# Performance work log

Measured on AMD Instinct MI355X. Metric: run time of the kernel, lower is better.

Reference implementation:

```python
import jax, jax.numpy as jnp
import numpy as np

EPS = 1e-5
K = 5


def _bn(h, g, b):
    # BatchNorm1d in training mode: batch stats over all dims except channels.
    ax = tuple(range(h.ndim - 1))
    mu = jnp.mean(h, axis=ax, keepdims=True)
    var = jnp.var(h, axis=ax, keepdims=True)
    return g * (h - mu) * jax.lax.rsqrt(var + EPS) + b


def _block(x, w, b, g, be):
    # Lin -> ReLU -> BN, as in MLP() helper
    return _bn(jax.nn.relu(x @ w + b), g, be)


def _knn_idx(x, k):
    # x: [B, P, D]; k nearest per point (includes self at distance 0)
    sq = jnp.sum(x * x, axis=-1)
    d2 = sq[:, :, None] + sq[:, None, :] - 2.0 * jnp.einsum('bpd,bqd->bpq', x, x)
    return jax.lax.top_k(-d2, k)[1]  # [B, P, k]


def _edge_conv(x, k, mlp_fn):
    # DynamicEdgeConv: recompute kNN graph on current features, gather
    # neighbor/center pairs, per-edge MLP on [x_i, x_j - x_i], max-aggregate.
    idx = _knn_idx(x, k)                                   # [B,P,k]
    xj = jax.vmap(lambda xb, ib: xb[ib])(x, idx)           # [B,P,k,D]
    xi = jnp.broadcast_to(x[:, :, None, :], xj.shape)
    e = jnp.concatenate([xi, xj - xi], axis=-1)            # [B,P,k,2D]
    return jnp.max(mlp_fn(e), axis=2)                      # max aggr -> [B,P,C]


def dec_forward(pos,
                c1w0, c1b0, c1g0, c1e0,
                c1w1, c1b1, c1g1, c1e1,
                c1w2, c1b2, c1g2, c1e2,
                c2w, c2b, c2g, c2e,
                l1w, l1b, l1g, l1e,
                m1w, m1b, m1g, m1e,
                m2w, m2b, m2g, m2e,
                m3w, m3b):
    mlp1 = lambda e: _block(_block(_block(e, c1w0, c1b0, c1g0, c1e0),
                                   c1w1, c1b1, c1g1, c1e1),
                            c1w2, c1b2, c1g2, c1e2)
    x1 = _edge_conv(pos, K, mlp1)                          # [B,P,64]
    x2 = _edge_conv(x1, K, lambda e: _block(e, c2w, c2b, c2g, c2e))  # [B,P,128]
    h = _block(jnp.concatenate([x1, x2], axis=-1), l1w, l1b, l1g, l1e)  # [B,P,1024]
    p = jnp.max(h, axis=1)                                 # global_max_pool -> [B,1024]
    p = _block(p, m1w, m1b, m1g, m1e)                      # dropout omitted (eval)
    p = _block(p, m2w, m2b, m2g, m2e)
    return p @ m3w + m3b                                   # [B, n_classes]


def setup_inputs() -> dict:
    key = jax.random.key(0)
    ks = jax.random.split(key, 12)
    B, P = 16, 2048

    def w(k, shape):
        return 0.05 * jax.random.normal(k, shape, jnp.float32)

    z = lambda c: jnp.zeros((c,), jnp.float32)
    o = lambda c: jnp.ones((c,), jnp.float32)

    d = {
        'pos': jax.random.normal(ks[0], (B, P, 3), jnp.float32),
        'c1w0': w(ks[1], (6, 64)), 'c1b0': z(64), 'c1g0': o(64), 'c1e0': z(64),
        'c1w1': w(ks[2], (64, 64)), 'c1b1': z(64), 'c1g1': o(64), 'c1e1': z(64),
        'c1w2': w(ks[3], (64, 64)), 'c1b2': z(64), 'c1g2': o(64), 'c1e2': z(64),
        'c2w': w(ks[4], (128, 128)), 'c2b': z(128), 'c2g': o(128), 'c2e': z(128),
        'l1w': w(ks[5], (192, 1024)), 'l1b': z(1024), 'l1g': o(1024), 'l1e': z(1024),
        'm1w': w(ks[6], (1024, 512)), 'm1b': z(512), 'm1g': o(512), 'm1e': z(512),
        'm2w': w(ks[7], (512, 256)), 'm2b': z(256), 'm2g': o(256), 'm2e': z(256),
        'm3w': w(ks[8], (256, 2)), 'm3b': z(2),
    }
    return d


def reference(pos,
              c1w0, c1b0, c1g0, c1e0,
              c1w1, c1b1, c1g1, c1e1,
              c1w2, c1b2, c1g2, c1e2,
              c2w, c2b, c2g, c2e,
              l1w, l1b, l1g, l1e,
              m1w, m1b, m1g, m1e,
              m2w, m2b, m2g, m2e,
              m3w, m3b):
    return dec_forward(pos,
                       c1w0, c1b0, c1g0, c1e0,
                       c1w1, c1b1, c1g1, c1e1,
                       c1w2, c1b2, c1g2, c1e2,
                       c2w, c2b, c2g, c2e,
                       l1w, l1b, l1g, l1e,
                       m1w, m1b, m1g, m1e,
                       m2w, m2b, m2g, m2e,
                       m3w, m3b)
```

## Files before the change

kernel.cpp:

```cpp
#include <hip/hip_runtime.h>
#include <cmath>

constexpr int B = 16, P = 2048, KNN = 5;
constexpr int BP = B * P;
constexpr int E = BP * KNN;
constexpr float EPS = 1e-5f;
constexpr int QC2 = 4;

constexpr int ST0 = 0;
constexpr int ST1 = 128;
constexpr int ST2 = 256;
constexpr int ST3 = 384;
constexpr int ST4 = 640;
constexpr int ST5 = 2688;
constexpr int ST6 = 3712;
constexpr int ST_TOTAL = 4224;

typedef __attribute__((ext_vector_type(8))) short bf16x8;
typedef __attribute__((ext_vector_type(4))) float f32x4;

__device__ inline unsigned short f2bf(float x) {
    unsigned u = __float_as_uint(x);
    unsigned r = (u + 0x7FFFu + ((u >> 16) & 1u)) >> 16;
    return (unsigned short)r;
}
__device__ inline void split2bf(float x, unsigned short& h, unsigned short& l) {
    unsigned short hh = f2bf(x);
    float fh = __uint_as_float(((unsigned)hh) << 16);
    h = hh;
    l = f2bf(x - fh);
}

__device__ inline void ins5(float d, int qi, float bd[KNN], int bi[KNN]) {
    bool c0 = d < bd[0], c1 = d < bd[1], c2 = d < bd[2], c3 = d < bd[3], c4 = d < bd[4];
    bd[4] = c3 ? bd[3] : (c4 ? d : bd[4]);  bi[4] = c3 ? bi[3] : (c4 ? qi : bi[4]);
    bd[3] = c2 ? bd[2] : (c3 ? d : bd[3]);  bi[3] = c2 ? bi[2] : (c3 ? qi : bi[3]);
    bd[2] = c1 ? bd[1] : (c2 ? d : bd[2]);  bi[2] = c1 ? bi[1] : (c2 ? qi : bi[2]);
    bd[1] = c0 ? bd[0] : (c1 ? d : bd[1]);  bi[1] = c0 ? bi[0] : (c1 ? qi : bi[1]);
    bd[0] = c0 ? d : bd[0];                 bi[0] = c0 ? qi : bi[0];
}
__device__ inline void ins5t(float d, int qi, float bd[KNN], int bi[KNN]) {
    bool c0 = (d < bd[0]) || (d == bd[0] && qi < bi[0]);
    bool c1 = (d < bd[1]) || (d == bd[1] && qi < bi[1]);
    bool c2 = (d < bd[2]) || (d == bd[2] && qi < bi[2]);
    bool c3 = (d < bd[3]) || (d == bd[3] && qi < bi[3]);
    bool c4 = (d < bd[4]) || (d == bd[4] && qi < bi[4]);
    bd[4] = c3 ? bd[3] : (c4 ? d : bd[4]);  bi[4] = c3 ? bi[3] : (c4 ? qi : bi[4]);
    bd[3] = c2 ? bd[2] : (c3 ? d : bd[3]);  bi[3] = c2 ? bi[2] : (c3 ? qi : bi[3]);
    bd[2] = c1 ? bd[1] : (c2 ? d : bd[2]);  bi[2] = c1 ? bi[1] : (c2 ? qi : bi[2]);
    bd[1] = c0 ? bd[0] : (c1 ? d : bd[1]);  bi[1] = c0 ? bi[0] : (c1 ? qi : bi[1]);
    bd[0] = c0 ? d : bd[0];                 bi[0] = c0 ? qi : bi[0];
}

__global__ void k_init(float* __restrict__ stats, float* __restrict__ pmax,
                       float* __restrict__ pmin) {
    int i = blockIdx.x * 256 + threadIdx.x;
    if (i < ST_TOTAL) stats[i] = 0.f;
    if (i < B * 1024) { pmax[i] = 0.f; pmin[i] = INFINITY; }
}

__global__ __launch_bounds__(256) void k_redstat(const float* __restrict__ part,
        float* __restrict__ stats, int nblk) {
    __shared__ float r[256];
    int slot = blockIdx.x;
    float s = 0.f;
    for (int i = threadIdx.x; i < nblk; i += 256)
        s += part[(size_t)i * 128 + slot];
    r[threadIdx.x] = s; __syncthreads();
    for (int o = 128; o; o >>= 1) {
        if (threadIdx.x < o) r[threadIdx.x] += r[threadIdx.x + o];
        __syncthreads();
    }
    if (threadIdx.x == 0) stats[slot] = r[0];
}

__global__ void k_wsplit(const float* __restrict__ w, unsigned short* __restrict__ th,
                         unsigned short* __restrict__ tl, int K, int N) {
    int i = blockIdx.x * 256 + threadIdx.x;
    if (i >= K * N) return;
    int k = i / N, n = i - k * N;
    float f = w[i];
    unsigned short h = f2bf(f);
    th[(size_t)n * K + k] = h;
    tl[(size_t)n * K + k] = f2bf(f - __uint_as_float((unsigned)h << 16));
}

__global__ void k_wprep2(const float* __restrict__ w,
        unsigned short* __restrict__ wdh, unsigned short* __restrict__ wdl,
        unsigned short* __restrict__ w1h, unsigned short* __restrict__ w1l) {
    int i = blockIdx.x * 256 + threadIdx.x;
    if (i >= 64 * 128) return;
    int k = i >> 7, n = i & 127;
    float w0 = w[k * 128 + n];
    float w1 = w[(64 + k) * 128 + n];
    float wd = w0 - w1;
    unsigned short h;
    h = f2bf(wd); wdh[n * 64 + k] = h;
    wdl[n * 64 + k] = f2bf(wd - __uint_as_float((unsigned)h << 16));
    h = f2bf(w1); w1h[n * 64 + k] = h;
    w1l[n * 64 + k] = f2bf(w1 - __uint_as_float((unsigned)h << 16));
}

__global__ void k_xsplit(const float* __restrict__ x, unsigned short* __restrict__ xh,
                         unsigned short* __restrict__ xl) {
    int i = blockIdx.x * 256 + threadIdx.x;
    float f = x[i];
    unsigned short h = f2bf(f);
    xh[i] = h;
    xl[i] = f2bf(f - __uint_as_float((unsigned)h << 16));
}

__global__ __launch_bounds__(256) void k_knn1(const float* __restrict__ pos,
                                              int* __restrict__ idx1) {
    __shared__ float4 qt[2048];
    int b = blockIdx.x >> 5;
    int p0 = (blockIdx.x & 31) << 6;
    const float* posb = pos + (size_t)b * P * 3;
#pragma unroll
    for (int t = 0; t < 8; ++t) {
        int q = (t << 8) + threadIdx.x;
        float qx = posb[q * 3 + 0], qy = posb[q * 3 + 1], qz = posb[q * 3 + 2];
        qt[q] = make_float4(qx, qy, qz, qx * qx + qy * qy + qz * qz);
    }
    __syncthreads();
    int pl = threadIdx.x >> 2, sub = threadIdx.x & 3;
    int p = p0 + pl;
    float4 me = qt[p];
    float x = me.x, y = me.y, z = me.z, sqp = me.w;
    float bd[KNN]; int bi[KNN];
#pragma unroll
    for (int i = 0; i < KNN; ++i) { bd[i] = INFINITY; bi[i] = 0; }
    for (int j0 = 0; j0 < 512; j0 += 8) {
        float4 v[8];
#pragma unroll
        for (int u = 0; u < 8; ++u) v[u] = qt[((j0 + u) << 2) | sub];
#pragma unroll
        for (int u = 0; u < 8; ++u) {
            float dot = x * v[u].x + y * v[u].y + z * v[u].z;
            float d2 = sqp + v[u].w - 2.f * dot;
            if (d2 < bd[KNN - 1]) ins5(d2, ((j0 + u) << 2) | sub, bd, bi);
        }
    }
#pragma unroll
    for (int w = 1; w <= 2; w <<= 1) {
        float od[KNN]; int oi[KNN];
#pragma unroll
        for (int i = 0; i < KNN; ++i) {
            od[i] = __shfl_xor(bd[i], w, 64);
            oi[i] = __shfl_xor(bi[i], w, 64);
        }
#pragma unroll
        for (int i = 0; i < KNN; ++i) ins5t(od[i], oi[i], bd, bi);
    }
    if (sub == 0) {
        size_t o = ((size_t)b * P + p) * KNN;
#pragma unroll
        for (int i = 0; i < KNN; ++i) idx1[o + i] = bi[i];
    }
}

__global__ __launch_bounds__(256) void k_ec1_l0(const float* __restrict__ pos,
        const int* __restrict__ idx1, const float* __restrict__ w,
        const float* __restrict__ bias, float* __restrict__ zout,
        float* __restrict__ part) {
    __shared__ float elds[256][6];
    __shared__ float red[256];
    int tid = threadIdx.x;
    int base = blockIdx.x * 256;
    {
        int e = base + tid;
        int bp = e / KNN;
        int bb = bp >> 11;
        int q = idx1[e];
        const float* pi = pos + (size_t)bp * 3;
        const float* pj = pos + ((size_t)(bb << 11) + q) * 3;
        float x0 = pi[0], x1v = pi[1], x2v = pi[2];
        elds[tid][0] = x0; elds[tid][1] = x1v; elds[tid][2] = x2v;
        elds[tid][3] = pj[0] - x0; elds[tid][4] = pj[1] - x1v; elds[tid][5] = pj[2] - x2v;
    }
    int c = tid & 63, lane = tid >> 6;
    float wr[6];
#pragma unroll
    for (int d = 0; d < 6; ++d) wr[d] = w[d * 64 + c];
    float bc = bias[c];
    __syncthreads();
    float s1 = 0.f, s2 = 0.f;
    for (int i = 0; i < 64; ++i) {
        int e = lane + (i << 2);
        float acc = bc;
#pragma unroll
        for (int d = 0; d < 6; ++d) acc = fmaf(elds[e][d], wr[d], acc);
        acc = fmaxf(acc, 0.f);
        zout[(size_t)(base + e) * 64 + c] = acc;
        s1 += acc; s2 = fmaf(acc, acc, s2);
    }
    red[tid] = s1; __syncthreads();
    if (tid < 64) part[(size_t)blockIdx.x * 128 + tid] =
        red[tid] + red[tid + 64] + red[tid + 128] + red[tid + 192];
    __syncthreads();
    red[tid] = s2; __syncthreads();
    if (tid < 64) part[(size_t)blockIdx.x * 128 + 64 + tid] =
        red[tid] + red[tid + 64] + red[tid + 128] + red[tid + 192];
}

__global__ __launch_bounds__(256) void k_lin64(const float* __restrict__ zin,
        const float* __restrict__ statsIn, const float* __restrict__ g,
        const float* __restrict__ be, const float* __restrict__ w,
        const float* __restrict__ bias, float* __restrict__ zout,
        float* __restrict__ part, float invN) {
    __shared__ __align__(16) float a[64 * 64];
    __shared__ float scl[64], shf[64];
    __shared__ float red[256];
    int tid = threadIdx.x;
    int base = blockIdx.x * 64;
    if (tid < 64) {
        float mu = statsIn[tid] * invN;
        float var = statsIn[64 + tid] * invN - mu * mu;
        float sc = g[tid] * rsqrtf(var + EPS);
        scl[tid] = sc; shf[tid] = be[tid] - mu * sc;
    }
    __syncthreads();
#pragma unroll
    for (int t = 0; t < 16; ++t) {
        int flat = tid + (t << 8);
        int k = flat & 63;
        a[flat] = fmaf(zin[(size_t)base * 64 + flat], scl[k], shf[k]);
    }
    int c = tid & 63, lane = tid >> 6;
    float wr[64];
#pragma unroll
    for (int k = 0; k < 64; ++k) wr[k] = w[k * 64 + c];
    float bc = bias[c];
    __syncthreads();
    float s1 = 0.f, s2 = 0.f;
    for (int i = 0; i < 16; ++i) {
        int e = lane + (i << 2);
        const float4* ap4 = (const float4*)(a + (e << 6));
        float acc = bc;
#pragma unroll
        for (int k4 = 0; k4 < 16; ++k4) {
            float4 v = ap4[k4];
            acc = fmaf(v.x, wr[k4 * 4 + 0], acc);
            acc = fmaf(v.y, wr[k4 * 4 + 1], acc);
            acc = fmaf(v.z, wr[k4 * 4 + 2], acc);
            acc = fmaf(v.w, wr[k4 * 4 + 3], acc);
        }
        acc = fmaxf(acc, 0.f);
        zout[(size_t)(base + e) * 64 + c] = acc;
        s1 += acc; s2 = fmaf(acc, acc, s2);
    }
    red[tid] = s1; __syncthreads();
    if (tid < 64) part[(size_t)blockIdx.x * 128 + tid] =
        red[tid] + red[tid + 64] + red[tid + 128] + red[tid + 192];
    __syncthreads();
    red[tid] = s2; __syncthreads();
    if (tid < 64) part[(size_t)blockIdx.x * 128 + 64 + tid] =
        red[tid] + red[tid + 64] + red[tid + 128] + red[tid + 192];
}

__global__ __launch_bounds__(256) void k_ec1_fin(const float* __restrict__ z2,
        const float* __restrict__ statsIn, const float* __restrict__ g,
        const float* __restrict__ be, float* __restrict__ x1,
        float* __restrict__ sq2) {
    int tid = threadIdx.x;
    int o = blockIdx.x * 256 + tid;
    int c = o & 63; int bp = o >> 6;
    float mu = statsIn[c] * (1.f / E);
    float var = statsIn[64 + c] * (1.f / E) - mu * mu;
    float sc = g[c] * rsqrtf(var + EPS);
    float sh = be[c] - mu * sc;
    float m = -INFINITY;
#pragma unroll
    for (int j = 0; j < KNN; ++j)
        m = fmaxf(m, fmaf(z2[((size_t)bp * KNN + j) * 64 + c], sc, sh));
    x1[o] = m;
    float ss = m * m;
#pragma unroll
    for (int off = 32; off; off >>= 1) ss += __shfl_down(ss, off, 64);
    if (c == 0) sq2[bp] = ss;
}

__global__ __launch_bounds__(128, 1) void k_knn2(const unsigned short* __restrict__ x1h,
        const unsigned short* __restrict__ x1l, const float* __restrict__ sq2,
        float* __restrict__ cd, int* __restrict__ ci) {
    __shared__ float S[2][32 * 129];
    int tid = threadIdx.x;
    int wv = tid >> 6, lane = tid & 63;
    int l15 = lane & 15, quad = lane >> 4;
    int qc = blockIdx.x & (QC2 - 1);
    int pt = blockIdx.x >> 2;
    int b = pt >> 5;
    int pw = ((pt & 31) << 6) + wv * 32;
    const size_t xbase = (size_t)b * P * 64;
    float* Sw = &S[wv][0];

    bf16x8 ah[2][2], al[2][2];
#pragma unroll
    for (int i = 0; i < 2; ++i)
#pragma unroll
        for (int kc = 0; kc < 2; ++kc) {
            size_t o = xbase + (size_t)(pw + i * 16 + l15) * 64 + kc * 32 + quad * 8;
            ah[i][kc] = *(const bf16x8*)&x1h[o];
            al[i][kc] = *(const bf16x8*)&x1l[o];
        }

    int half = lane >> 5;
    int pidx = lane & 31;
    float bd[KNN]; int bi[KNN];
#pragma unroll
    for (int i = 0; i < KNN; ++i) { bd[i] = INFINITY; bi[i] = 0; }

    int qlo = qc << 9;
    for (int t = 0; t < 4; ++t) {
        int q0 = qlo + (t << 7);
        float qsv[8];
#pragma unroll
        for (int j = 0; j < 8; ++j) qsv[j] = sq2[b * P + q0 + j * 16 + l15];
        f32x4 acc[2][8];
#pragma unroll
        for (int i = 0; i < 2; ++i)
#pragma unroll
            for (int j = 0; j < 8; ++j) acc[i][j] = (f32x4)0.f;
#pragma unroll
        for (int kc = 0; kc < 2; ++kc) {
            bf16x8 bh[8], bl[8];
#pragma unroll
            for (int j = 0; j < 8; ++j) {
                size_t o = xbase + (size_t)(q0 + j * 16 + l15) * 64 + kc * 32 + quad * 8;
                bh[j] = *(const bf16x8*)&x1h[o];
                bl[j] = *(const bf16x8*)&x1l[o];
            }
#pragma unroll
            for (int i = 0; i < 2; ++i)
#pragma unroll
                for (int j = 0; j < 8; ++j) {
                    acc[i][j] = __builtin_amdgcn_mfma_f32_16x16x32_bf16(ah[i][kc], bh[j], acc[i][j], 0, 0, 0);
                    acc[i][j] = __builtin_amdgcn_mfma_f32_16x16x32_bf16(ah[i][kc], bl[j], acc[i][j], 0, 0, 0);
                    acc[i][j] = __builtin_amdgcn_mfma_f32_16x16x32_bf16(al[i][kc], bh[j], acc[i][j], 0, 0, 0);
                }
        }
#pragma unroll
        for (int i = 0; i < 2; ++i)
#pragma unroll
            for (int j = 0; j < 8; ++j)
#pragma unroll
                for (int r = 0; r < 4; ++r) {
                    int pl = i * 16 + quad * 4 + r;
                    Sw[pl * 129 + j * 16 + l15] = fmaf(acc[i][j][r], -2.f, qsv[j]);
                }
        const float* row = Sw + pidx * 129 + half * 64;
        int qb = q0 + half * 64;
        for (int jj = 0; jj < 64; jj += 4) {
            float k0 = row[jj + 0], k1 = row[jj + 1], k2 = row[jj + 2], k3 = row[jj + 3];
            if (k0 < bd[4]) ins5(k0, qb + jj + 0, bd, bi);
            if (k1 < bd[4]) ins5(k1, qb + jj + 1, bd, bi);
            if (k2 < bd[4]) ins5(k2, qb + jj + 2, bd, bi);
            if (k3 < bd[4]) ins5(k3, qb + jj + 3, bd, bi);
        }
    }
#pragma unroll
    for (int i = 0; i < KNN; ++i) {
        float od = __shfl_xor(bd[i], 32, 64);
        int oi = __shfl_xor(bi[i], 32, 64);
        if (half == 0) ins5t(od, oi, bd, bi);
    }
    if (half == 0) {
        size_t o = (((size_t)b * P + pw + pidx) * QC2 + qc) * KNN;
#pragma unroll
        for (int i = 0; i < KNN; ++i) { cd[o + i] = bd[i]; ci[o + i] = bi[i]; }
    }
}

__global__ __launch_bounds__(256) void k_knn2m(const float* __restrict__ cd,
        const int* __restrict__ ci, int* __restrict__ idx2) {
    int bp = blockIdx.x * 256 + threadIdx.x;
    float bd[KNN]; int bi[KNN];
#pragma unroll
    for (int i = 0; i < KNN; ++i) { bd[i] = INFINITY; bi[i] = 0; }
    size_t o = (size_t)bp * QC2 * KNN;
    for (int t = 0; t < QC2 * KNN; ++t) {
        float d2 = cd[o + t]; int qi = ci[o + t];
        if (d2 < bd[KNN - 1]) ins5(d2, qi, bd, bi);
    }
#pragma unroll
    for (int i = 0; i < KNN; ++i) idx2[bp * KNN + i] = bi[i];
}

__global__ __launch_bounds__(256) void k_ec2m(
        const unsigned short* __restrict__ x1h, const unsigned short* __restrict__ x1l,
        const int* __restrict__ idx2,
        const unsigned short* __restrict__ wdh, const unsigned short* __restrict__ wdl,
        const unsigned short* __restrict__ w1h, const unsigned short* __restrict__ w1l,
        const float* __restrict__ bias, float* __restrict__ zout,
        float* __restrict__ stats) {
    __shared__ float red[2 * 128 * 2];
    int tid = threadIdx.x;
    int base = blockIdx.x * 128;
    int bb = base / (P * KNN);
    int wv = tid >> 6, lane = tid & 63;
    int wm = wv >> 1, wn = wv & 1;
    int l15 = lane & 15, quad = lane >> 4;
    int rI[4], rJ[4];
#pragma unroll
    for (int i = 0; i < 4; ++i) {
        int e = base + wm * 64 + i * 16 + l15;
        rI[i] = e / KNN;
        rJ[i] = (bb << 11) + idx2[e];
    }
    f32x4 acc[4][4];
#pragma unroll
    for (int i = 0; i < 4; ++i)
#pragma unroll
        for (int j = 0; j < 4; ++j) acc[i][j] = (f32x4)0.f;

#pragma unroll
    for (int s = 0; s < 2; ++s) {
        const unsigned short* bh_ = s ? w1h : wdh;
        const unsigned short* bl_ = s ? w1l : wdl;
#pragma unroll
        for (int kc = 0; kc < 2; ++kc) {
            bf16x8 afh[4], afl[4], bfh[4], bfl[4];
#pragma unroll
            for (int i = 0; i < 4; ++i) {
                int row = s ? rJ[i] : rI[i];
                size_t o = (size_t)row * 64 + kc * 32 + quad * 8;
                afh[i] = *(const bf16x8*)&x1h[o];
                afl[i] = *(const bf16x8*)&x1l[o];
            }
#pragma unroll
            for (int j = 0; j < 4; ++j) {
                size_t wo = (size_t)(wn * 64 + j * 16 + l15) * 64 + kc * 32 + quad * 8;
                bfh[j] = *(const bf16x8*)&bh_[wo];
                bfl[j] = *(const bf16x8*)&bl_[wo];
            }
#pragma unroll
            for (int i = 0; i < 4; ++i)
#pragma unroll
                for (int j = 0; j < 4; ++j) {
                    acc[i][j] = __builtin_amdgcn_mfma_f32_16x16x32_bf16(afh[i], bfh[j], acc[i][j], 0, 0, 0);
                    acc[i][j] = __builtin_amdgcn_mfma_f32_16x16x32_bf16(afh[i], bfl[j], acc[i][j], 0, 0, 0);
                    acc[i][j] = __builtin_amdgcn_mfma_f32_16x16x32_bf16(afl[i], bfh[j], acc[i][j], 0, 0, 0);
                }
        }
    }
#pragma unroll
    for (int j = 0; j < 4; ++j) {
        int colL = wn * 64 + j * 16 + l15;
        float bl = bias[colL];
        float s1 = 0.f, s2 = 0.f;
#pragma unroll
        for (int i = 0; i < 4; ++i) {
            int row = wm * 64 + i * 16 + quad * 4;
#pragma unroll
            for (int r = 0; r < 4; ++r) {
                float v = fmaxf(acc[i][j][r] + bl, 0.f);
                zout[(size_t)(base + row + r) * 128 + colL] = v;
                s1 += v; s2 = fmaf(v, v, s2);
            }
        }
        s1 += __shfl_xor(s1, 16, 64); s1 += __shfl_xor(s1, 32, 64);
        s2 += __shfl_xor(s2, 16, 64); s2 += __shfl_xor(s2, 32, 64);
        if (quad == 0) {
            red[(wm * 128 + colL) * 2 + 0] = s1;
            red[(wm * 128 + colL) * 2 + 1] = s2;
        }
    }
    __syncthreads();
    if (tid < 128) {
        atomicAdd(&stats[tid], red[tid * 2] + red[(128 + tid) * 2]);
        atomicAdd(&stats[128 + tid], red[tid * 2 + 1] + red[(128 + tid) * 2 + 1]);
    }
}

__global__ __launch_bounds__(256) void k_ec2_fin(const float* __restrict__ z3,
        const float* __restrict__ stats, const float* __restrict__ g,
        const float* __restrict__ be, float* __restrict__ x2) {
    int o = blockIdx.x * 256 + threadIdx.x;
    int c = o & 127; int bp = o >> 7;
    float mu = stats[c] * (1.f / E);
    float var = stats[128 + c] * (1.f / E) - mu * mu;
    float sc = g[c] * rsqrtf(var + EPS);
    float sh = be[c] - mu * sc;
    float m = -INFINITY;
#pragma unroll
    for (int j = 0; j < KNN; ++j)
        m = fmaxf(m, fmaf(z3[((size_t)bp * KNN + j) * 128 + c], sc, sh));
    x2[o] = m;
}

__global__ __launch_bounds__(256) void k_l1m(
        const unsigned short* __restrict__ x1h, const unsigned short* __restrict__ x1l,
        const unsigned short* __restrict__ x2h, const unsigned short* __restrict__ x2l,
        const unsigned short* __restrict__ wth, const unsigned short* __restrict__ wtl,
        const float* __restrict__ bias, float* __restrict__ stats,
        float* __restrict__ pmax, float* __restrict__ pmin) {
    __shared__ float red[2 * 128 * 4];
    int tid = threadIdx.x;
    int brow = blockIdx.x & 255;
    int bcol = blockIdx.x >> 8;
    int row0 = brow << 7, col0 = bcol << 7;
    int wv = tid >> 6, lane = tid & 63;
    int wm = wv >> 1, wn = wv & 1;
    int l15 = lane & 15, quad = lane >> 4;
    f32x4 acc[4][4];
#pragma unroll
    for (int i = 0; i < 4; ++i)
#pragma unroll
        for (int j = 0; j < 4; ++j) acc[i][j] = (f32x4)0.f;

#pragma unroll
    for (int k0 = 0; k0 < 192; k0 += 32) {
        const unsigned short* ah = (k0 < 64) ? x1h : x2h;
        const unsigned short* al = (k0 < 64) ? x1l : x2l;
        int astr = (k0 < 64) ? 64 : 128;
        int aoff = (k0 < 64) ? k0 : (k0 - 64);
        bf16x8 afh[4], afl[4], bfh[4], bfl[4];
#pragma unroll
        for (int i = 0; i < 4; ++i) {
            size_t o = (size_t)(row0 + wm * 64 + i * 16 + l15) * astr + aoff + quad * 8;
            afh[i] = *(const bf16x8*)&ah[o];
            afl[i] = *(const bf16x8*)&al[o];
        }
#pragma unroll
        for (int j = 0; j < 4; ++j) {
            size_t wo = (size_t)(col0 + wn * 64 + j * 16 + l15) * 192 + k0 + quad * 8;
            bfh[j] = *(const bf16x8*)&wth[wo];
            bfl[j] = *(const bf16x8*)&wtl[wo];
        }
#pragma unroll
        for (int i = 0; i < 4; ++i)
#pragma unroll
            for (int j = 0; j < 4; ++j) {
                acc[i][j] = __builtin_amdgcn_mfma_f32_16x16x32_bf16(afh[i], bfh[j], acc[i][j], 0, 0, 0);
                acc[i][j] = __builtin_amdgcn_mfma_f32_16x16x32_bf16(afh[i], bfl[j], acc[i][j], 0, 0, 0);
                acc[i][j] = __builtin_amdgcn_mfma_f32_16x16x32_bf16(afl[i], bfh[j], acc[i][j], 0, 0, 0);
            }
    }
#pragma unroll
    for (int j = 0; j < 4; ++j) {
        int colL = wn * 64 + j * 16 + l15;
        float bl = bias[col0 + colL];
        float s1 = 0.f, s2 = 0.f, mx = 0.f, mn = INFINITY;
#pragma unroll
        for (int i = 0; i < 4; ++i)
#pragma unroll
            for (int r = 0; r < 4; ++r) {
                float v = fmaxf(acc[i][j][r] + bl, 0.f);
                s1 += v; s2 = fmaf(v, v, s2);
                mx = fmaxf(mx, v); mn = fminf(mn, v);
            }
        s1 += __shfl_xor(s1, 16, 64); s1 += __shfl_xor(s1, 32, 64);
        s2 += __shfl_xor(s2, 16, 64); s2 += __shfl_xor(s2, 32, 64);
        mx = fmaxf(mx, __shfl_xor(mx, 16, 64)); mx = fmaxf(mx, __shfl_xor(mx, 32, 64));
        mn = fminf(mn, __shfl_xor(mn, 16, 64)); mn = fminf(mn, __shfl_xor(mn, 32, 64));
        if (quad == 0) {
            float* rp = &red[(wm * 128 + colL) * 4];
            rp[0] = s1; rp[1] = s2; rp[2] = mx; rp[3] = mn;
        }
    }
    __syncthreads();
    if (tid < 128) {
        const float* r0 = &red[tid * 4];
        const float* r1 = &red[(128 + tid) * 4];
        int bb = row0 >> 11;
        atomicAdd(&stats[col0 + tid], r0[0] + r1[0]);
        atomicAdd(&stats[1024 + col0 + tid], r0[1] + r1[1]);
        atomicMax((unsigned int*)&pmax[bb * 1024 + col0 + tid],
                  __float_as_uint(fmaxf(r0[2], r1[2])));
        atomicMin((unsigned int*)&pmin[bb * 1024 + col0 + tid],
                  __float_as_uint(fminf(r0[3], r1[3])));
    }
}

__global__ void k_pool(const float* __restrict__ stats, const float* __restrict__ g,
                       const float* __restrict__ be, const float* __restrict__ pmax,
                       const float* __restrict__ pmin, float* __restrict__ p) {
    int o = blockIdx.x * 256 + threadIdx.x;
    int c = o & 1023;
    float mu = stats[c] * (1.f / BP);
    float var = stats[1024 + c] * (1.f / BP) - mu * mu;
    float sc = g[c] * rsqrtf(var + EPS);
    float sh = be[c] - mu * sc;
    float v = (sc >= 0.f) ? pmax[o] : pmin[o];
    p[o] = fmaf(v, sc, sh);
}

__global__ __launch_bounds__(256) void k_m1(const float* __restrict__ p,
        const float* __restrict__ w, const float* __restrict__ bias,
        float* __restrict__ t1, float* __restrict__ stats) {
    int o = blockIdx.x * 256 + threadIdx.x;
    int c = o & 511, b = o >> 9;
    const float* pr = p + (b << 10);
    float acc = bias[c];
    for (int k = 0; k < 1024; ++k) acc = fmaf(pr[k], w[k * 512 + c], acc);
    acc = fmaxf(acc, 0.f);
    t1[o] = acc;
    atomicAdd(&stats[c], acc);
    atomicAdd(&stats[512 + c], acc * acc);
}

__global__ __launch_bounds__(256) void k_m2(const float* __restrict__ t1,
        const float* __restrict__ stats5, const float* __restrict__ g,
        const float* __restrict__ be, const float* __restrict__ w,
        const float* __restrict__ bias, float* __restrict__ t2,
        float* __restrict__ stats6) {
    __shared__ float scl[512], shf[512];
    int tid = threadIdx.x;
    for (int t = tid; t < 512; t += 256) {
        float mu = stats5[t] * (1.f / 16.f);
        float var = stats5[512 + t] * (1.f / 16.f) - mu * mu;
        float sc = g[t] * rsqrtf(var + EPS);
        scl[t] = sc; shf[t] = be[t] - mu * sc;
    }
    __syncthreads();
    int o = blockIdx.x * 256 + tid;
    int c = o & 255, b = o >> 8;
    const float* tr = t1 + (b << 9);
    float acc = bias[c];
    for (int k = 0; k < 512; ++k) {
        float u = fmaf(tr[k], scl[k], shf[k]);
        acc = fmaf(u, w[k * 256 + c], acc);
    }
    acc = fmaxf(acc, 0.f);
    t2[o] = acc;
    atomicAdd(&stats6[c], acc);
    atomicAdd(&stats6[256 + c], acc * acc);
}

__global__ __launch_bounds__(256) void k_m3(const float* __restrict__ t2,
        const float* __restrict__ stats6, const float* __restrict__ g,
        const float* __restrict__ be, const float* __restrict__ w,
        const float* __restrict__ bias, float* __restrict__ out) {
    __shared__ float scl[256], shf[256];
    int tid = threadIdx.x;
    {
        float mu = stats6[tid] * (1.f / 16.f);
        float var = stats6[256 + tid] * (1.f / 16.f) - mu * mu;
        float sc = g[tid] * rsqrtf(var + EPS);
        scl[tid] = sc; shf[tid] = be[tid] - mu * sc;
    }
    __syncthreads();
    if (tid < 32) {
        int c = tid & 1, b = tid >> 1;
        const float* tr = t2 + (b << 8);
        float acc = bias[c];
        for (int k = 0; k < 256; ++k) {
            float u = fmaf(tr[k], scl[k], shf[k]);
            acc = fmaf(u, w[k * 2 + c], acc);
        }
        out[tid] = acc;
    }
}

extern "C" void kernel_launch(void* const* d_in, const int* in_sizes, int n_in,
                              void* d_out, int out_size, void* d_ws, size_t ws_size,
                              hipStream_t stream) {
    const float* pos  = (const float*)d_in[0];
    const float* c1w0 = (const float*)d_in[1];
    const float* c1b0 = (const float*)d_in[2];
    const float* c1g0 = (const float*)d_in[3];
    const float* c1e0 = (const float*)d_in[4];
    const float* c1w1 = (const float*)d_in[5];
    const float* c1b1 = (const float*)d_in[6];
    const float* c1g1 = (const float*)d_in[7];
    const float* c1e1 = (const float*)d_in[8];
    const float* c1w2 = (const float*)d_in[9];
    const float* c1b2 = (const float*)d_in[10];
    const float* c1g2 = (const float*)d_in[11];
    const float* c1e2 = (const float*)d_in[12];
    const float* c2w  = (const float*)d_in[13];
    const float* c2b  = (const float*)d_in[14];
    const float* c2g  = (const float*)d_in[15];
    const float* c2e  = (const float*)d_in[16];
    const float* l1w  = (const float*)d_in[17];
    const float* l1b  = (const float*)d_in[18];
    const float* l1g  = (const float*)d_in[19];
    const float* l1e  = (const float*)d_in[20];
    const float* m1w  = (const float*)d_in[21];
    const float* m1b  = (const float*)d_in[22];
    const float* m1g  = (const float*)d_in[23];
    const float* m1e  = (const float*)d_in[24];
    const float* m2w  = (const float*)d_in[25];
    const float* m2b  = (const float*)d_in[26];
    const float* m2g  = (const float*)d_in[27];
    const float* m2e  = (const float*)d_in[28];
    const float* m3w  = (const float*)d_in[29];
    const float* m3b  = (const float*)d_in[30];
    float* out = (float*)d_out;

    char* ws = (char*)d_ws;
    size_t off = 0;
    auto alloc = [&](size_t bytes) {
        size_t r = off; off = (off + bytes + 255) & ~(size_t)255; return r;
    };
    float* stats = (float*)(ws + alloc(ST_TOTAL * 4));
    float* pmax  = (float*)(ws + alloc(16 * 1024 * 4));
    float* pmin  = (float*)(ws + alloc(16 * 1024 * 4));
    float* pbuf  = (float*)(ws + alloc(16 * 1024 * 4));
    float* t1    = (float*)(ws + alloc(16 * 512 * 4));
    float* t2    = (float*)(ws + alloc(16 * 256 * 4));
    float* sq2   = (float*)(ws + alloc((size_t)BP * 4));
    float* part  = (float*)(ws + alloc((size_t)(E / 64) * 128 * 4));
    unsigned short* wthL = (unsigned short*)(ws + alloc((size_t)192 * 1024 * 2));
    unsigned short* wtlL = (unsigned short*)(ws + alloc((size_t)192 * 1024 * 2));
    unsigned short* wdh  = (unsigned short*)(ws + alloc((size_t)128 * 64 * 2));
    unsigned short* wdl  = (unsigned short*)(ws + alloc((size_t)128 * 64 * 2));
    unsigned short* w1h  = (unsigned short*)(ws + alloc((size_t)128 * 64 * 2));
    unsigned short* w1l  = (unsigned short*)(ws + alloc((size_t)128 * 64 * 2));
    int*   idx1  = (int*)  (ws + alloc((size_t)E * 4));
    int*   idx2  = (int*)  (ws + alloc((size_t)E * 4));
    float* x1    = (float*)(ws + alloc((size_t)BP * 64 * 4));
    float* x2    = (float*)(ws + alloc((size_t)BP * 128 * 4));
    float* zA    = (float*)(ws + alloc((size_t)E * 128 * 4));
    float* zB    = (float*)(ws + alloc((size_t)E * 64 * 4));
    unsigned short* x1h = (unsigned short*)zB;
    unsigned short* x1l = x1h + (size_t)BP * 64;
    float* cand_d = (float*)(x1l + (size_t)BP * 64);
    int*   cand_i = (int*)(cand_d + (size_t)BP * QC2 * KNN);
    unsigned short* x2h = (unsigned short*)(cand_i + (size_t)BP * QC2 * KNN);
    unsigned short* x2l = x2h + (size_t)BP * 128;

    (void)in_sizes; (void)n_in; (void)out_size; (void)ws_size;

    k_init<<<64, 256, 0, stream>>>(stats, pmax, pmin);
    k_wsplit<<<(192 * 1024 + 255) / 256, 256, 0, stream>>>(l1w, wthL, wtlL, 192, 1024);
    k_wprep2<<<(64 * 128 + 255) / 256, 256, 0, stream>>>(c2w, wdh, wdl, w1h, w1l);
    k_knn1<<<B * 32, 256, 0, stream>>>(pos, idx1);
    k_ec1_l0<<<E / 256, 256, 0, stream>>>(pos, idx1, c1w0, c1b0, zA, part);
    k_redstat<<<128, 256, 0, stream>>>(part, stats + ST0, E / 256);
    k_lin64<<<E / 64, 256, 0, stream>>>(zA, stats + ST0, c1g0, c1e0, c1w1, c1b1,
                                        zB, part, 1.f / E);
    k_redstat<<<128, 256, 0, stream>>>(part, stats + ST1, E / 64);
    k_lin64<<<E / 64, 256, 0, stream>>>(zB, stats + ST1, c1g1, c1e1, c1w2, c1b2,
                                        zA, part, 1.f / E);
    k_redstat<<<128, 256, 0, stream>>>(part, stats + ST2, E / 64);
    k_ec1_fin<<<BP * 64 / 256, 256, 0, stream>>>(zA, stats + ST2, c1g2, c1e2, x1, sq2);
    k_xsplit<<<BP * 64 / 256, 256, 0, stream>>>(x1, x1h, x1l);
    k_knn2<<<B * 32 * QC2, 128, 0, stream>>>(x1h, x1l, sq2, cand_d, cand_i);
    k_knn2m<<<BP / 256, 256, 0, stream>>>(cand_d, cand_i, idx2);
    k_ec2m<<<E / 128, 256, 0, stream>>>(x1h, x1l, idx2, wdh, wdl, w1h, w1l,
                                        c2b, zA, stats + ST3);
    k_ec2_fin<<<BP * 128 / 256, 256, 0, stream>>>(zA, stats + ST3, c2g, c2e, x2);
    k_xsplit<<<BP * 128 / 256, 256, 0, stream>>>(x2, x2h, x2l);
    k_l1m<<<256 * 8, 256, 0, stream>>>(x1h, x1l, x2h, x2l, wthL, wtlL, l1b,
                                       stats + ST4, pmax, pmin);
    k_pool<<<64, 256, 0, stream>>>(stats + ST4, l1g, l1e, pmax, pmin, pbuf);
    k_m1<<<32, 256, 0, stream>>>(pbuf, m1w, m1b, t1, stats + ST5);
    k_m2<<<16, 256, 0, stream>>>(t1, stats + ST5, m1g, m1e, m2w, m2b, t2, stats + ST6);
    k_m3<<<1, 256, 0, stream>>>(t2, stats + ST6, m2g, m2e, m3w, m3b, out);
}
```

Baseline: 648.3 us.

## Fold BN into weights and run edge MLP layers on bf16x3 MFMA

Replaces the scalar FP32 64x64 linear layers of the first edge conv with MFMA-based kernels using a split-bf16 (hi/lo) three-product scheme. The BatchNorm scale and shift are folded into the next layer's weights and bias by a small prep kernel. Intermediate activations are stored as bf16 hi/lo pairs instead of fp32. The aim is to cut the FP32 ALU cost of the per-edge MLP, at the price of an extra tiny kernel per layer and a slight precision change from the split representation.

```diff
diff --git a/kernel.cpp b/kernel.cpp
--- a/kernel.cpp
+++ b/kernel.cpp
@@ -24,11 +24,13 @@
     unsigned r = (u + 0x7FFFu + ((u >> 16) & 1u)) >> 16;
     return (unsigned short)r;
 }
+__device__ inline float bf2f(unsigned short h) {
+    return __uint_as_float(((unsigned)h) << 16);
+}
 __device__ inline void split2bf(float x, unsigned short& h, unsigned short& l) {
     unsigned short hh = f2bf(x);
-    float fh = __uint_as_float(((unsigned)hh) << 16);
     h = hh;
-    l = f2bf(x - fh);
+    l = f2bf(x - bf2f(hh));
 }
 
 __device__ inline void ins5(float d, int qi, float bd[KNN], int bi[KNN]) {
@@ -82,7 +84,31 @@
     float f = w[i];
     unsigned short h = f2bf(f);
     th[(size_t)n * K + k] = h;
-    tl[(size_t)n * K + k] = f2bf(f - __uint_as_float((unsigned)h << 16));
+    tl[(size_t)n * K + k] = f2bf(f - bf2f(h));
+}
+
+__global__ __launch_bounds__(64) void k_wfold(const float* __restrict__ stats,
+        const float* __restrict__ g, const float* __restrict__ be,
+        const float* __restrict__ w, const float* __restrict__ bias,
+        unsigned short* __restrict__ wfh, unsigned short* __restrict__ wfl,
+        float* __restrict__ bias2, float invN) {
+    __shared__ float red[64];
+    int n = blockIdx.x, k = threadIdx.x;
+    float mu = stats[k] * invN;
+    float var = stats[64 + k] * invN - mu * mu;
+    float sc = g[k] * rsqrtf(var + EPS);
+    float sh = be[k] - mu * sc;
+    float wv = w[k * 64 + n];
+    float wf = sc * wv;
+    unsigned short h, l;
+    split2bf(wf, h, l);
+    wfh[n * 64 + k] = h; wfl[n * 64 + k] = l;
+    red[k] = sh * wv; __syncthreads();
+    for (int o = 32; o; o >>= 1) {
+        if (k < o) red[k] += red[k + o];
+        __syncthreads();
+    }
+    if (k == 0) bias2[n] = bias[n] + red[0];
 }
 
 __global__ void k_wprep2(const float* __restrict__ w,
@@ -94,20 +120,18 @@
     float w0 = w[k * 128 + n];
     float w1 = w[(64 + k) * 128 + n];
     float wd = w0 - w1;
-    unsigned short h;
-    h = f2bf(wd); wdh[n * 64 + k] = h;
-    wdl[n * 64 + k] = f2bf(wd - __uint_as_float((unsigned)h << 16));
-    h = f2bf(w1); w1h[n * 64 + k] = h;
-    w1l[n * 64 + k] = f2bf(w1 - __uint_as_float((unsigned)h << 16));
+    unsigned short h, l;
+    split2bf(wd, h, l); wdh[n * 64 + k] = h; wdl[n * 64 + k] = l;
+    split2bf(w1, h, l); w1h[n * 64 + k] = h; w1l[n * 64 + k] = l;
 }
 
 __global__ void k_xsplit(const float* __restrict__ x, unsigned short* __restrict__ xh,
                          unsigned short* __restrict__ xl) {
     int i = blockIdx.x * 256 + threadIdx.x;
     float f = x[i];
-    unsigned short h = f2bf(f);
-    xh[i] = h;
-    xl[i] = f2bf(f - __uint_as_float((unsigned)h << 16));
+    unsigned short h, l;
+    split2bf(f, h, l);
+    xh[i] = h; xl[i] = l;
 }
 
 __global__ __launch_bounds__(256) void k_knn1(const float* __restrict__ pos,
@@ -161,8 +185,8 @@
 
 __global__ __launch_bounds__(256) void k_ec1_l0(const float* __restrict__ pos,
         const int* __restrict__ idx1, const float* __restrict__ w,
-        const float* __restrict__ bias, float* __restrict__ zout,
-        float* __restrict__ part) {
+        const float* __restrict__ bias, unsigned short* __restrict__ zh,
+        unsigned short* __restrict__ zl, float* __restrict__ part) {
     __shared__ float elds[256][6];
     __shared__ float red[256];
     int tid = threadIdx.x;
@@ -191,7 +215,10 @@
 #pragma unroll
         for (int d = 0; d < 6; ++d) acc = fmaf(elds[e][d], wr[d], acc);
         acc = fmaxf(acc, 0.f);
-        zout[(size_t)(base + e) * 64 + c] = acc;
+        unsigned short h, l;
+        split2bf(acc, h, l);
+        zh[(size_t)(base + e) * 64 + c] = h;
+        zl[(size_t)(base + e) * 64 + c] = l;
         s1 += acc; s2 = fmaf(acc, acc, s2);
     }
     red[tid] = s1; __syncthreads();
@@ -203,62 +230,82 @@
         red[tid] + red[tid + 64] + red[tid + 128] + red[tid + 192];
 }
 
-__global__ __launch_bounds__(256) void k_lin64(const float* __restrict__ zin,
-        const float* __restrict__ statsIn, const float* __restrict__ g,
-        const float* __restrict__ be, const float* __restrict__ w,
-        const float* __restrict__ bias, float* __restrict__ zout,
-        float* __restrict__ part, float invN) {
-    __shared__ __align__(16) float a[64 * 64];
-    __shared__ float scl[64], shf[64];
-    __shared__ float red[256];
+__global__ __launch_bounds__(128) void k_lin64m(
+        const unsigned short* __restrict__ zinh, const unsigned short* __restrict__ zinl,
+        const unsigned short* __restrict__ wfh, const unsigned short* __restrict__ wfl,
+        const float* __restrict__ bias2, unsigned short* __restrict__ zouth,
+        unsigned short* __restrict__ zoutl, float* __restrict__ part) {
+    __shared__ float red[2 * 64 * 2];
     int tid = threadIdx.x;
-    int base = blockIdx.x * 64;
+    int wv = tid >> 6, lane = tid & 63;
+    int l15 = lane & 15, quad = lane >> 4;
+    int row0 = blockIdx.x * 128 + wv * 64;
+    f32x4 acc[4][4];
+#pragma unroll
+    for (int i = 0; i < 4; ++i)
+#pragma unroll
+        for (int j = 0; j < 4; ++j) acc[i][j] = (f32x4)0.f;
+
+#pragma unroll
+    for (int kc = 0; kc < 2; ++kc) {
+        bf16x8 afh[4], afl[4], bfh[4], bfl[4];
+#pragma unroll
+        for (int i = 0; i < 4; ++i) {
+            size_t o = (size_t)(row0 + i * 16 + l15) * 64 + kc * 32 + quad * 8;
+            afh[i] = *(const bf16x8*)&zinh[o];
+            afl[i] = *(const bf16x8*)&zinl[o];
+        }
+#pragma unroll
+        for (int j = 0; j < 4; ++j) {
+            size_t wo = (size_t)(j * 16 + l15) * 64 + kc * 32 + quad * 8;
+            bfh[j] = *(const bf16x8*)&wfh[wo];
+            bfl[j] = *(const bf16x8*)&wfl[wo];
+        }
+#pragma unroll
+        for (int i = 0; i < 4; ++i)
+#pragma unroll
+            for (int j = 0; j < 4; ++j) {
+                acc[i][j] = __builtin_amdgcn_mfma_f32_16x16x32_bf16(afh[i], bfh[j], acc[i][j], 0, 0, 0);
+                acc[i][j] = __builtin_amdgcn_mfma_f32_16x16x32_bf16(afh[i], bfl[j], acc[i][j], 0, 0, 0);
+                acc[i][j] = __builtin_amdgcn_mfma_f32_16x16x32_bf16(afl[i], bfh[j], acc[i][j], 0, 0, 0);
+            }
+    }
+#pragma unroll
+    for (int j = 0; j < 4; ++j) {
+        int colL = j * 16 + l15;
+        float bl = bias2[colL];
+        float s1 = 0.f, s2 = 0.f;
+#pragma unroll
+        for (int i = 0; i < 4; ++i) {
+            int row = row0 + i * 16 + quad * 4;
+#pragma unroll
+            for (int r = 0; r < 4; ++r) {
+                float v = fmaxf(acc[i][j][r] + bl, 0.f);
+                unsigned short h, l;
+                split2bf(v, h, l);
+                zouth[(size_t)(row + r) * 64 + colL] = h;
+                zoutl[(size_t)(row + r) * 64 + colL] = l;
+                s1 += v; s2 = fmaf(v, v, s2);
+            }
+        }
+        s1 += __shfl_xor(s1, 16, 64); s1 += __shfl_xor(s1, 32, 64);
+        s2 += __shfl_xor(s2, 16, 64); s2 += __shfl_xor(s2, 32, 64);
+        if (quad == 0) {
+            red[(wv * 64 + colL) * 2 + 0] = s1;
+            red[(wv * 64 + colL) * 2 + 1] = s2;
+        }
+    }
+    __syncthreads();
     if (tid < 64) {
-        float mu = statsIn[tid] * invN;
-        float var = statsIn[64 + tid] * invN - mu * mu;
-        float sc = g[tid] * rsqrtf(var + EPS);
-        scl[tid] = sc; shf[tid] = be[tid] - mu * sc;
-    }
-    __syncthreads();
-#pragma unroll
-    for (int t = 0; t < 16; ++t) {
-        int flat = tid + (t << 8);
-        int k = flat & 63;
-        a[flat] = fmaf(zin[(size_t)base * 64 + flat], scl[k], shf[k]);
-    }
-    int c = tid & 63, lane = tid >> 6;
-    float wr[64];
-#pragma unroll
-    for (int k = 0; k < 64; ++k) wr[k] = w[k * 64 + c];
-    float bc = bias[c];
-    __syncthreads();
-    float s1 = 0.f, s2 = 0.f;
-    for (int i = 0; i < 16; ++i) {
-        int e = lane + (i << 2);
-        const float4* ap4 = (const float4*)(a + (e << 6));
-        float acc = bc;
-#pragma unroll
-        for (int k4 = 0; k4 < 16; ++k4) {
-            float4 v = ap4[k4];
-            acc = fmaf(v.x, wr[k4 * 4 + 0], acc);
-            acc = fmaf(v.y, wr[k4 * 4 + 1], acc);
-            acc = fmaf(v.z, wr[k4 * 4 + 2], acc);
-            acc = fmaf(v.w, wr[k4 * 4 + 3], acc);
-        }
-        acc = fmaxf(acc, 0.f);
-        zout[(size_t)(base + e) * 64 + c] = acc;
-        s1 += acc; s2 = fmaf(acc, acc, s2);
-    }
-    red[tid] = s1; __syncthreads();
-    if (tid < 64) part[(size_t)blockIdx.x * 128 + tid] =
-        red[tid] + red[tid + 64] + red[tid + 128] + red[tid + 192];
-    __syncthreads();
-    red[tid] = s2; __syncthreads();
-    if (tid < 64) part[(size_t)blockIdx.x * 128 + 64 + tid] =
-        red[tid] + red[tid + 64] + red[tid + 128] + red[tid + 192];
-}
-
-__global__ __launch_bounds__(256) void k_ec1_fin(const float* __restrict__ z2,
+        part[(size_t)blockIdx.x * 128 + tid] =
+            red[tid * 2] + red[(64 + tid) * 2];
+        part[(size_t)blockIdx.x * 128 + 64 + tid] =
+            red[tid * 2 + 1] + red[(64 + tid) * 2 + 1];
+    }
+}
+
+__global__ __launch_bounds__(256) void k_ec1_fin(const unsigned short* __restrict__ z2h,
+        const unsigned short* __restrict__ z2l,
         const float* __restrict__ statsIn, const float* __restrict__ g,
         const float* __restrict__ be, float* __restrict__ x1,
         float* __restrict__ sq2) {
@@ -271,8 +318,11 @@
     float sh = be[c] - mu * sc;
     float m = -INFINITY;
 #pragma unroll
-    for (int j = 0; j < KNN; ++j)
-        m = fmaxf(m, fmaf(z2[((size_t)bp * KNN + j) * 64 + c], sc, sh));
+    for (int j = 0; j < KNN; ++j) {
+        size_t zo = ((size_t)bp * KNN + j) * 64 + c;
+        float v = bf2f(z2h[zo]) + bf2f(z2l[zo]);
+        m = fmaxf(m, fmaf(v, sc, sh));
+    }
     x1[o] = m;
     float ss = m * m;
 #pragma unroll
@@ -707,12 +757,24 @@
     unsigned short* wdl  = (unsigned short*)(ws + alloc((size_t)128 * 64 * 2));
     unsigned short* w1h  = (unsigned short*)(ws + alloc((size_t)128 * 64 * 2));
     unsigned short* w1l  = (unsigned short*)(ws + alloc((size_t)128 * 64 * 2));
+    unsigned short* wf1h = (unsigned short*)(ws + alloc((size_t)64 * 64 * 2));
+    unsigned short* wf1l = (unsigned short*)(ws + alloc((size_t)64 * 64 * 2));
+    unsigned short* wf2h = (unsigned short*)(ws + alloc((size_t)64 * 64 * 2));
+    unsigned short* wf2l = (unsigned short*)(ws + alloc((size_t)64 * 64 * 2));
+    float* bias2a = (float*)(ws + alloc(64 * 4));
+    float* bias2b = (float*)(ws + alloc(64 * 4));
     int*   idx1  = (int*)  (ws + alloc((size_t)E * 4));
     int*   idx2  = (int*)  (ws + alloc((size_t)E * 4));
     float* x1    = (float*)(ws + alloc((size_t)BP * 64 * 4));
     float* x2    = (float*)(ws + alloc((size_t)BP * 128 * 4));
     float* zA    = (float*)(ws + alloc((size_t)E * 128 * 4));
     float* zB    = (float*)(ws + alloc((size_t)E * 64 * 4));
+    unsigned short* z0h = (unsigned short*)zA;
+    unsigned short* z0l = z0h + (size_t)E * 64;
+    unsigned short* z1h = z0l + (size_t)E * 64;
+    unsigned short* z1l = z1h + (size_t)E * 64;
+    unsigned short* z2h = (unsigned short*)zB;
+    unsigned short* z2l = z2h + (size_t)E * 64;
     unsigned short* x1h = (unsigned short*)zB;
     unsigned short* x1l = x1h + (size_t)BP * 64;
     float* cand_d = (float*)(x1l + (size_t)BP * 64);
@@ -726,15 +788,20 @@
     k_wsplit<<<(192 * 1024 + 255) / 256, 256, 0, stream>>>(l1w, wthL, wtlL, 192, 1024);
     k_wprep2<<<(64 * 128 + 255) / 256, 256, 0, stream>>>(c2w, wdh, wdl, w1h, w1l);
     k_knn1<<<B * 32, 256, 0, stream>>>(pos, idx1);
-    k_ec1_l0<<<E / 256, 256, 0, stream>>>(pos, idx1, c1w0, c1b0, zA, part);
+    k_ec1_l0<<<E / 256, 256, 0, stream>>>(pos, idx1, c1w0, c1b0, z0h, z0l, part);
     k_redstat<<<128, 256, 0, stream>>>(part, stats + ST0, E / 256);
-    k_lin64<<<E / 64, 256, 0, stream>>>(zA, stats + ST0, c1g0, c1e0, c1w1, c1b1,
-                                        zB, part, 1.f / E);
-    k_redstat<<<128, 256, 0, stream>>>(part, stats + ST1, E / 64);
-    k_lin64<<<E / 64, 256, 0, stream>>>(zB, stats + ST1, c1g1, c1e1, c1w2, c1b2,
-                                        zA, part, 1.f / E);
-    k_redstat<<<128, 256, 0, stream>>>(part, stats + ST2, E / 64);
-    k_ec1_fin<<<BP * 64 / 256, 256, 0, stream>>>(zA, stats + ST2, c1g2, c1e2, x1, sq2);
+    k_wfold<<<64, 64, 0, stream>>>(stats + ST0, c1g0, c1e0, c1w1, c1b1,
+                                   wf1h, wf1l, bias2a, 1.f / E);
+    k_lin64m<<<E / 128, 128, 0, stream>>>(z0h, z0l, wf1h, wf1l, bias2a,
+                                          z1h, z1l, part);
+    k_redstat<<<128, 256, 0, stream>>>(part, stats + ST1, E / 128);
+    k_wfold<<<64, 64, 0, stream>>>(stats + ST1, c1g1, c1e1, c1w2, c1b2,
+                                   wf2h, wf2l, bias2b, 1.f / E);
+    k_lin64m<<<E / 128, 128, 0, stream>>>(z1h, z1l, wf2h, wf2l, bias2b,
+                                          z2h, z2l, part);
+    k_redstat<<<128, 256, 0, stream>>>(part, stats + ST2, E / 128);
+    k_ec1_fin<<<BP * 64 / 256, 256, 0, stream>>>(z2h, z2l, stats + ST2, c1g2, c1e2,
+                                                 x1, sq2);
     k_xsplit<<<BP * 64 / 256, 256, 0, stream>>>(x1, x1h, x1l);
     k_knn2<<<B * 32 * QC2, 128, 0, stream>>>(x1h, x1l, sq2, cand_d, cand_i);
     k_knn2m<<<BP / 256, 256, 0, stream>>>(cand_d, cand_i, idx2);
```

Result: no change. 660.2 us (+1.8%).
